# Performance work log

Hardware: AMD Instinct MI355X
Metric: run time of the kernel (lower is better)

The kernel has to match this reference:

```python
import jax, jax.numpy as jnp
import numpy as np

STRIDE = 1

def setup_inputs() -> dict:
    key = jax.random.key(0)
    k1, k2 = jax.random.split(key)
    x = jax.random.normal(k1, (16, 32, 32768), dtype=jnp.float32)
    # original uses torch.rand -> uniform [0,1)
    kernel = jax.random.uniform(k2, (1, 32, 32, 3), dtype=jnp.float32)
    return {"x": x, "kernel": kernel}

def reference(x, kernel):
    # Faithful intent of the module: strided valid 1D convolution.
    # x: (B, C_in, L); kernel: (1, C_out, C_in, K)
    w = kernel[0]  # (C_out, C_in, K)
    out = jax.lax.conv_general_dilated(
        x, w,
        window_strides=(STRIDE,),
        padding='VALID',
        dimension_numbers=('NCH', 'OIH', 'NCH'),
    )  # (B, C_out, (L-K)//STRIDE + 1)
    return out
```

## Files before the change

### kernel.cpp

```cpp
#include <hip/hip_runtime.h>

#define L_IN   32768
#define L_OUT  32766
#define C_IN   32
#define C_OUT  32
#define KW     3
#define TILE_L 128
#define TPB    4
#define NGRP   64
#define XROWS  130
#define PITCHW 32
#define LDSW   (XROWS * PITCHW)
#define WPLANE 3072

typedef __attribute__((ext_vector_type(8))) short bf16x8;
typedef __attribute__((ext_vector_type(4))) float f32x4;
typedef __attribute__((ext_vector_type(4))) unsigned int u32x4;

__device__ __forceinline__ unsigned pack_split(float v) {
    unsigned u = __float_as_uint(v);
    unsigned r = u + 0x7fffu + ((u >> 16) & 1u);
    float lo = v - __uint_as_float(r & 0xffff0000u);
    return (__float_as_uint(lo) & 0xffff0000u) | (r >> 16);
}

__device__ __forceinline__ int lds_word(int l, int ci) {
    return l * PITCHW + ((((ci >> 2) ^ (l & 7)) << 2) | (ci & 3));
}

__global__ void prep_w(const float* __restrict__ w, unsigned short* __restrict__ wtf) {
    const int i = blockIdx.x * 256 + threadIdx.x;
    if (i >= 6 * 64 * 8) return;
    const int f    = i >> 9;
    const int rr   = i & 511;
    const int lane = rr >> 3;
    const int j    = rr & 7;
    const int kw   = f >> 1;
    const int cot  = f & 1;
    const int co   = cot * 16 + (lane & 15);
    const int ci   = (lane >> 4) * 8 + j;
    const float v  = w[(co * C_IN + ci) * KW + kw];
    unsigned u = __float_as_uint(v);
    unsigned r = u + 0x7fffu + ((u >> 16) & 1u);
    unsigned short hi = (unsigned short)(r >> 16);
    float lof = v - __uint_as_float(r & 0xffff0000u);
    unsigned lu = __float_as_uint(lof);
    unsigned lr = lu + 0x7fffu + ((lu >> 16) & 1u);
    unsigned short lo = (unsigned short)(lr >> 16);
    wtf[(f * 64 + lane) * 8 + j]          = hi;
    wtf[WPLANE + (f * 64 + lane) * 8 + j] = lo;
}

__global__ __launch_bounds__(256, 4) void conv1d_mfma(
    const float* __restrict__ x, const unsigned short* __restrict__ wtf,
    float* __restrict__ out)
{
    __shared__ __attribute__((aligned(16))) unsigned       xs[LDSW];
    __shared__ __attribute__((aligned(16))) unsigned short wl[2 * WPLANE];

    const int tid  = threadIdx.x;
    const int lane = tid & 63;
    const int wv   = tid >> 6;
    const int bb   = blockIdx.x >> 6;
    const int grp  = blockIdx.x & (NGRP - 1);
    const int lg0  = grp * (TILE_L * TPB);

    const float* xb = x + (size_t)bb * C_IN * L_IN;

    {
        const u32x4* wsv = (const u32x4*)wtf;
        u32x4*       wdv = (u32x4*)wl;
#pragma unroll
        for (int i = 0; i < 3; ++i)
            wdv[tid * 3 + i] = wsv[tid * 3 + i];
    }

    const int c   = tid & 31;
    const int rr0 = tid >> 5;
    const int n   = lane & 15;
    const int kg  = lane >> 4;
    const int lb  = wv * 32;

    float sv[2][4][4];
    float hv[2];

    auto LOADT = [&](int l0, int s) {
#pragma unroll
        for (int r = 0; r < 4; ++r) {
            const float* src = xb + (size_t)(rr0 + r * 8) * L_IN + l0;
#pragma unroll
            for (int q = 0; q < 4; ++q)
                sv[s][r][q] = src[c + q * 32];
        }
        hv[s] = 0.f;
        if (tid < 64) {
            const int gl = l0 + TILE_L + (tid & 1);
            if (gl < L_IN) hv[s] = xb[(size_t)(tid >> 1) * L_IN + gl];
        }
        asm volatile("" ::: "memory");
    };
    auto WRITET = [&](int s) {
#pragma unroll
        for (int r = 0; r < 4; ++r)
#pragma unroll
            for (int q = 0; q < 4; ++q)
                xs[lds_word(c + q * 32, rr0 + r * 8)] = pack_split(sv[s][r][q]);
        if (tid < 64)
            xs[lds_word(TILE_L + (tid & 1), tid >> 1)] = pack_split(hv[s]);
    };

    LOADT(lg0, 0);
    LOADT(lg0 + TILE_L, 1);

    float* ob = out + (size_t)bb * C_OUT * L_OUT;

#pragma unroll
    for (int t = 0; t < TPB; ++t) {
        const int l0 = lg0 + t * TILE_L;
        WRITET(t & 1);
        if (t + 2 < TPB) LOADT(l0 + 2 * TILE_L, t & 1);
        __syncthreads();

        f32x4 acc[2][2];
#pragma unroll
        for (int a = 0; a < 2; ++a)
#pragma unroll
            for (int bq = 0; bq < 2; ++bq)
                acc[a][bq] = (f32x4){0.f, 0.f, 0.f, 0.f};

#pragma unroll
        for (int kw = 0; kw < KW; ++kw) {
            const int f0 = kw * 2, f1 = kw * 2 + 1;
            const bf16x8 ah0 = *(const bf16x8*)&wl[(f0 * 64 + lane) * 8];
            const bf16x8 al0 = *(const bf16x8*)&wl[WPLANE + (f0 * 64 + lane) * 8];
            const bf16x8 ah1 = *(const bf16x8*)&wl[(f1 * 64 + lane) * 8];
            const bf16x8 al1 = *(const bf16x8*)&wl[WPLANE + (f1 * 64 + lane) * 8];
#pragma unroll
            for (int lt = 0; lt < 2; ++lt) {
                const int lrow = lb + lt * 16 + n + kw;
                const int base = lrow * PITCHW;
                const int sw   = lrow & 7;
                const u32x4 pa = *(const u32x4*)&xs[base + (((kg * 2 + 0) ^ sw) << 2)];
                const u32x4 pb = *(const u32x4*)&xs[base + (((kg * 2 + 1) ^ sw) << 2)];
                u32x4 BH, BL;
                BH[0] = (pa[0] & 0xffffu) | (pa[1] << 16);
                BH[1] = (pa[2] & 0xffffu) | (pa[3] << 16);
                BH[2] = (pb[0] & 0xffffu) | (pb[1] << 16);
                BH[3] = (pb[2] & 0xffffu) | (pb[3] << 16);
                BL[0] = (pa[0] >> 16) | (pa[1] & 0xffff0000u);
                BL[1] = (pa[2] >> 16) | (pa[3] & 0xffff0000u);
                BL[2] = (pb[0] >> 16) | (pb[1] & 0xffff0000u);
                BL[3] = (pb[2] >> 16) | (pb[3] & 0xffff0000u);
                const bf16x8 bh = __builtin_bit_cast(bf16x8, BH);
                const bf16x8 bl = __builtin_bit_cast(bf16x8, BL);

                acc[0][lt] = __builtin_amdgcn_mfma_f32_16x16x32_bf16(ah0, bh, acc[0][lt], 0, 0, 0);
                acc[0][lt] = __builtin_amdgcn_mfma_f32_16x16x32_bf16(ah0, bl, acc[0][lt], 0, 0, 0);
                acc[0][lt] = __builtin_amdgcn_mfma_f32_16x16x32_bf16(al0, bh, acc[0][lt], 0, 0, 0);
                acc[1][lt] = __builtin_amdgcn_mfma_f32_16x16x32_bf16(ah1, bh, acc[1][lt], 0, 0, 0);
                acc[1][lt] = __builtin_amdgcn_mfma_f32_16x16x32_bf16(ah1, bl, acc[1][lt], 0, 0, 0);
                acc[1][lt] = __builtin_amdgcn_mfma_f32_16x16x32_bf16(al1, bh, acc[1][lt], 0, 0, 0);
            }
        }

        const int lw = l0 + lb;
        if (lw + 31 < L_OUT) {
#pragma unroll
            for (int cot = 0; cot < 2; ++cot)
#pragma unroll
                for (int lt = 0; lt < 2; ++lt) {
                    float* op = ob + (size_t)(cot * 16 + kg * 4) * L_OUT + lw + lt * 16 + n;
#pragma unroll
                    for (int r = 0; r < 4; ++r)
                        op[(size_t)r * L_OUT] = acc[cot][lt][r];
                }
        } else {
#pragma unroll
            for (int cot = 0; cot < 2; ++cot)
#pragma unroll
                for (int lt = 0; lt < 2; ++lt) {
                    const int l = lw + lt * 16 + n;
                    if (l < L_OUT) {
                        float* op = ob + (size_t)(cot * 16 + kg * 4) * L_OUT + l;
#pragma unroll
                        for (int r = 0; r < 4; ++r)
                            op[(size_t)r * L_OUT] = acc[cot][lt][r];
                    }
                }
        }

        if (t + 1 < TPB) __syncthreads();
    }
}

extern "C" void kernel_launch(void* const* d_in, const int* in_sizes, int n_in,
                              void* d_out, int out_size, void* d_ws, size_t ws_size,
                              hipStream_t stream) {
    const float* x = (const float*)d_in[0];
    const float* w = (const float*)d_in[1];
    float* out     = (float*)d_out;
    unsigned short* wtf = (unsigned short*)d_ws;

    prep_w<<<dim3(12), 256, 0, stream>>>(w, wtf);
    conv1d_mfma<<<dim3(16 * NGRP), 256, 0, stream>>>(x, wtf, out);
}
```

Before: 119.1 us.

## Give each wave a private LDS tile to drop block barriers, use v_perm packing

Each wave now loads and stages only its own 32-column slice plus a 2-column halo into a private LDS region, so the per-tile __syncthreads calls are removed and only one barrier after the weight copy remains. Global loads become float2 per lane over channel rows instead of scalar loads. The bf16 hi/lo unpacking switches from shift/mask sequences to v_perm_b32. The cost is redundant halo loads per wave and a different, possibly less coalesced global access pattern, and correctness now relies on wave-level execution ordering for LDS reuse without barriers.

```diff
diff --git a/kernel.cpp b/kernel.cpp
--- a/kernel.cpp
+++ b/kernel.cpp
@@ -8,9 +8,8 @@
 #define TILE_L 128
 #define TPB    4
 #define NGRP   64
-#define XROWS  130
+#define WCOLS  34
 #define PITCHW 32
-#define LDSW   (XROWS * PITCHW)
 #define WPLANE 3072
 
 typedef __attribute__((ext_vector_type(8))) short bf16x8;
@@ -24,8 +23,12 @@
     return (__float_as_uint(lo) & 0xffff0000u) | (r >> 16);
 }
 
-__device__ __forceinline__ int lds_word(int l, int ci) {
-    return l * PITCHW + ((((ci >> 2) ^ (l & 7)) << 2) | (ci & 3));
+__device__ __forceinline__ unsigned prm(unsigned hi, unsigned lo, unsigned sel) {
+    return __builtin_amdgcn_perm(hi, lo, sel);
+}
+
+__device__ __forceinline__ int lds_word(int col, int ci) {
+    return col * PITCHW + ((((ci >> 2) ^ (col & 7)) << 2) | (ci & 3));
 }
 
 __global__ void prep_w(const float* __restrict__ w, unsigned short* __restrict__ wtf) {
@@ -55,8 +58,8 @@
     const float* __restrict__ x, const unsigned short* __restrict__ wtf,
     float* __restrict__ out)
 {
-    __shared__ __attribute__((aligned(16))) unsigned       xs[LDSW];
-    __shared__ __attribute__((aligned(16))) unsigned short wl[2 * WPLANE];
+    __shared__ __attribute__((aligned(16))) unsigned       xsl[4 * WCOLS * PITCHW];
+    __shared__ __attribute__((aligned(16))) unsigned short wlds[2 * WPLANE];
 
     const int tid  = threadIdx.x;
     const int lane = tid & 63;
@@ -69,48 +72,52 @@
 
     {
         const u32x4* wsv = (const u32x4*)wtf;
-        u32x4*       wdv = (u32x4*)wl;
+        u32x4*       wdv = (u32x4*)wlds;
 #pragma unroll
         for (int i = 0; i < 3; ++i)
             wdv[tid * 3 + i] = wsv[tid * 3 + i];
     }
 
-    const int c   = tid & 31;
-    const int rr0 = tid >> 5;
-    const int n   = lane & 15;
-    const int kg  = lane >> 4;
-    const int lb  = wv * 32;
-
-    float sv[2][4][4];
-    float hv[2];
-
-    auto LOADT = [&](int l0, int s) {
-#pragma unroll
-        for (int r = 0; r < 4; ++r) {
-            const float* src = xb + (size_t)(rr0 + r * 8) * L_IN + l0;
-#pragma unroll
-            for (int q = 0; q < 4; ++q)
-                sv[s][r][q] = src[c + q * 32];
-        }
-        hv[s] = 0.f;
-        if (tid < 64) {
-            const int gl = l0 + TILE_L + (tid & 1);
-            if (gl < L_IN) hv[s] = xb[(size_t)(tid >> 1) * L_IN + gl];
+    const int n  = lane & 15;
+    const int kg = lane >> 4;
+    const int lb = wv * 32;
+
+    unsigned* xw = xsl + wv * (WCOLS * PITCHW);
+
+    float2 sv[2][8];
+    float2 hv[2];
+
+    auto LOADT = [&](int l0w, int s) {
+#pragma unroll
+        for (int r = 0; r < 8; ++r) {
+            const int ci = kg + r * 4;
+            sv[s][r] = *(const float2*)(xb + (size_t)ci * L_IN + l0w + 2 * n);
+        }
+        hv[s] = make_float2(0.f, 0.f);
+        if (lane < 32) {
+            const int gl = l0w + 32;
+            if (gl + 1 < L_IN)
+                hv[s] = *(const float2*)(xb + (size_t)lane * L_IN + gl);
         }
         asm volatile("" ::: "memory");
     };
     auto WRITET = [&](int s) {
 #pragma unroll
-        for (int r = 0; r < 4; ++r)
-#pragma unroll
-            for (int q = 0; q < 4; ++q)
-                xs[lds_word(c + q * 32, rr0 + r * 8)] = pack_split(sv[s][r][q]);
-        if (tid < 64)
-            xs[lds_word(TILE_L + (tid & 1), tid >> 1)] = pack_split(hv[s]);
+        for (int r = 0; r < 8; ++r) {
+            const int ci = kg + r * 4;
+            const int c0 = 2 * n, c1 = 2 * n + 1;
+            xw[lds_word(c0, ci)] = pack_split(sv[s][r].x);
+            xw[lds_word(c1, ci)] = pack_split(sv[s][r].y);
+        }
+        if (lane < 32) {
+            xw[lds_word(32, lane)] = pack_split(hv[s].x);
+            xw[lds_word(33, lane)] = pack_split(hv[s].y);
+        }
     };
 
-    LOADT(lg0, 0);
-    LOADT(lg0 + TILE_L, 1);
+    LOADT(lg0 + lb, 0);
+    LOADT(lg0 + lb + TILE_L, 1);
+    __syncthreads();
 
     float* ob = out + (size_t)bb * C_OUT * L_OUT;
 
@@ -118,8 +125,7 @@
     for (int t = 0; t < TPB; ++t) {
         const int l0 = lg0 + t * TILE_L;
         WRITET(t & 1);
-        if (t + 2 < TPB) LOADT(l0 + 2 * TILE_L, t & 1);
-        __syncthreads();
+        if (t + 2 < TPB) LOADT(lg0 + lb + (t + 2) * TILE_L, t & 1);
 
         f32x4 acc[2][2];
 #pragma unroll
@@ -131,26 +137,26 @@
 #pragma unroll
         for (int kw = 0; kw < KW; ++kw) {
             const int f0 = kw * 2, f1 = kw * 2 + 1;
-            const bf16x8 ah0 = *(const bf16x8*)&wl[(f0 * 64 + lane) * 8];
-            const bf16x8 al0 = *(const bf16x8*)&wl[WPLANE + (f0 * 64 + lane) * 8];
-            const bf16x8 ah1 = *(const bf16x8*)&wl[(f1 * 64 + lane) * 8];
-            const bf16x8 al1 = *(const bf16x8*)&wl[WPLANE + (f1 * 64 + lane) * 8];
+            const bf16x8 ah0 = *(const bf16x8*)&wlds[(f0 * 64 + lane) * 8];
+            const bf16x8 al0 = *(const bf16x8*)&wlds[WPLANE + (f0 * 64 + lane) * 8];
+            const bf16x8 ah1 = *(const bf16x8*)&wlds[(f1 * 64 + lane) * 8];
+            const bf16x8 al1 = *(const bf16x8*)&wlds[WPLANE + (f1 * 64 + lane) * 8];
 #pragma unroll
             for (int lt = 0; lt < 2; ++lt) {
-                const int lrow = lb + lt * 16 + n + kw;
+                const int lrow = lt * 16 + n + kw;
                 const int base = lrow * PITCHW;
                 const int sw   = lrow & 7;
-                const u32x4 pa = *(const u32x4*)&xs[base + (((kg * 2 + 0) ^ sw) << 2)];
-                const u32x4 pb = *(const u32x4*)&xs[base + (((kg * 2 + 1) ^ sw) << 2)];
+                const u32x4 pa = *(const u32x4*)&xw[base + (((kg * 2 + 0) ^ sw) << 2)];
+                const u32x4 pb = *(const u32x4*)&xw[base + (((kg * 2 + 1) ^ sw) << 2)];
                 u32x4 BH, BL;
-                BH[0] = (pa[0] & 0xffffu) | (pa[1] << 16);
-                BH[1] = (pa[2] & 0xffffu) | (pa[3] << 16);
-                BH[2] = (pb[0] & 0xffffu) | (pb[1] << 16);
-                BH[3] = (pb[2] & 0xffffu) | (pb[3] << 16);
-                BL[0] = (pa[0] >> 16) | (pa[1] & 0xffff0000u);
-                BL[1] = (pa[2] >> 16) | (pa[3] & 0xffff0000u);
-                BL[2] = (pb[0] >> 16) | (pb[1] & 0xffff0000u);
-                BL[3] = (pb[2] >> 16) | (pb[3] & 0xffff0000u);
+                BH[0] = prm(pa[1], pa[0], 0x05040100u);
+                BH[1] = prm(pa[3], pa[2], 0x05040100u);
+                BH[2] = prm(pb[1], pb[0], 0x05040100u);
+                BH[3] = prm(pb[3], pb[2], 0x05040100u);
+                BL[0] = prm(pa[1], pa[0], 0x07060302u);
+                BL[1] = prm(pa[3], pa[2], 0x07060302u);
+                BL[2] = prm(pb[1], pb[0], 0x07060302u);
+                BL[3] = prm(pb[3], pb[2], 0x07060302u);
                 const bf16x8 bh = __builtin_bit_cast(bf16x8, BH);
                 const bf16x8 bl = __builtin_bit_cast(bf16x8, BL);
 
@@ -188,8 +194,6 @@
                     }
                 }
         }
-
-        if (t + 1 < TPB) __syncthreads();
     }
 }
 
```

Measured after the change: 129.9 us. 1.09x slower.
